# Optimization experiments

Hardware: AMD Instinct MI355X
Metric: run time of the kernel (lower is better)

Reference implementation:

```python
import jax, jax.numpy as jnp
import numpy as np

N = 8192      # num nodes
D = 128       # feature dim (input_dim)
E = 262144    # num edges (avg degree 32)
P = 4         # num perspectives (num_pers)
EPSILON = 0.3 # similarity threshold (args.epsilon)


def setup_inputs() -> dict:
    key = jax.random.key(0)
    k1, k2, k3, k4 = jax.random.split(key, 4)
    x = jax.random.normal(k1, (N, D), dtype=jnp.float32)
    ori_index = jax.random.randint(k2, (2, E), 0, N, dtype=jnp.int32)
    ori_weight = jax.random.uniform(k3, (E,), dtype=jnp.float32)
    w_pers = jax.random.normal(k4, (P, D), dtype=jnp.float32)  # weighted-cosine perspective weights
    return {"x": x, "ori_index": ori_index, "ori_weight": ori_weight, "w_pers": w_pers}


def reference(x, ori_index, ori_weight, w_pers):
    n = x.shape[0]
    # to_dense_adj: scatter edge weights into dense [N, N] adjacency (duplicate edges add)
    ori_g = jnp.zeros((n, n), dtype=x.dtype).at[ori_index[0], ori_index[1]].add(ori_weight)

    # GraphLearner (weighted multi-perspective cosine):
    # reweight features per perspective, L2-normalize, cosine sim, mean over perspectives
    xw = x[None, :, :] * w_pers[:, None, :]                              # [P, N, D]
    xn = xw / jnp.maximum(jnp.linalg.norm(xw, axis=-1, keepdims=True), 1e-12)
    sim = jnp.mean(jnp.einsum('pnd,pmd->pnm', xn, xn), axis=0)           # [N, N]
    # epsilon-thresholded learned graph
    sim_g = jnp.where(sim > EPSILON, sim, jnp.zeros_like(sim))

    # purified(sim, ori_g, epsilon): keep original edges where sim*ori_g > epsilon
    pur_g = jnp.where(sim * ori_g > EPSILON, ori_g, jnp.zeros_like(sim))
    new_g = pur_g + sim_g
    # dense_to_sparse has data-dependent output size; return the dense refined
    # adjacency (same information: edges = nonzero(new_g), weights = values).
    return new_g
```

## Files before the change

kernel.cpp:

```cpp
#include <hip/hip_runtime.h>
#include <hip/hip_bf16.h>
#include <stdint.h>

#define N_NODES 8192
#define DIM     128
#define KTOT    512
#define NEDGE   262144
#define EPS     0.3f
#define FIX_DELTA 0.008f
#define FIX_CAP (1u << 19)
#define XCAP    (1u << 18)
#define LCAP    512
#define HASH_BITS 19
#define HASH_SLOTS (1u << HASH_BITS)

typedef unsigned int u32;
typedef unsigned short u16;
typedef __attribute__((ext_vector_type(8))) short short8;
typedef __attribute__((ext_vector_type(4))) float float4v;

#define OFF_YF  0u
#define OFF_YB  16777216u
#define OFF_CTR 25165824u
#define OFF_HK  25166080u
#define OFF_HV  27263232u
#define OFF_FL  29360384u
#define OFF_UL  31457536u
#define OFF_XL  32506112u
#define MEMSET_OFF OFF_CTR
#define MEMSET_BYTES (OFF_FL - OFF_CTR)

__device__ __forceinline__ u16 f2bf(float f) {
    u32 b = __builtin_bit_cast(u32, f);
    b += 0x7fffu + ((b >> 16) & 1u);
    return (u16)(b >> 16);
}

__global__ void prep_y(const float* __restrict__ x, const float* __restrict__ wp,
                       float* __restrict__ yf, u16* __restrict__ yb) {
    int node = blockIdx.x * 4 + (threadIdx.x >> 6);
    int lane = threadIdx.x & 63;
    float x0 = x[node * DIM + lane];
    float x1 = x[node * DIM + lane + 64];
    for (int p = 0; p < 4; ++p) {
        float v0 = x0 * wp[p * DIM + lane];
        float v1 = x1 * wp[p * DIM + lane + 64];
        float ss = v0 * v0 + v1 * v1;
        #pragma unroll
        for (int o = 1; o < 64; o <<= 1) ss += __shfl_xor(ss, o, 64);
        float scale = 0.5f / fmaxf(sqrtf(ss), 1e-12f);
        float y0 = v0 * scale, y1 = v1 * scale;
        int base = node * KTOT + p * DIM;
        yf[base + lane] = y0;       yf[base + lane + 64] = y1;
        yb[base + lane] = f2bf(y0); yb[base + lane + 64] = f2bf(y1);
    }
}

__global__ void edge_insert(const int* __restrict__ idx, const float* __restrict__ w,
                            u32* __restrict__ hkey, float* __restrict__ hval,
                            u32* __restrict__ ucnt, u32* __restrict__ ulist) {
    int e = blockIdx.x * 256 + threadIdx.x;
    u32 cell = (u32)(idx[e] * N_NODES + idx[NEDGE + e]);
    float wv = w[e];
    u32 key = cell + 1u;
    u32 h = (cell * 2654435761u) >> (32 - HASH_BITS);
    while (true) {
        u32 old = atomicCAS(&hkey[h], 0u, key);
        if (old == 0u) { ulist[atomicAdd(ucnt, 1u)] = h; atomicAdd(&hval[h], wv); break; }
        if (old == key) { atomicAdd(&hval[h], wv); break; }
        h = (h + 1u) & (HASH_SLOTS - 1u);
    }
}

#define TM  128
#define BK  64
#define TLD 132

__global__ __launch_bounds__(512)
void gemm_sim(const u16* __restrict__ yb, float* __restrict__ out,
              u32* __restrict__ fcnt, u32* __restrict__ flst) {
    int bm = blockIdx.y, bn = blockIdx.x;
    if (bm > bn) return;
    __shared__ __align__(16) char smem[64 * TLD * 4];
    u16* As = (u16*)smem;
    u16* Bs = As + TM * BK;
    float* tbuf = (float*)smem;
    __shared__ u32 s_cnt, s_base;
    __shared__ u32 s_list[LCAP];
    int tid = threadIdx.x;
    int lane = tid & 63, wid = tid >> 6;
    int wm = wid >> 1, wn = wid & 1;
    if (tid == 0) s_cnt = 0;

    float4v acc[2][4] = {};
    const u16* arow = yb + (size_t)(bm * TM) * KTOT;
    const u16* brow = yb + (size_t)(bn * TM) * KTOT;

    for (int kt = 0; kt < KTOT / BK; ++kt) {
        __syncthreads();
        #pragma unroll
        for (int q = 0; q < 2; ++q) {
            int c = q * 512 + wid * 64 + lane;
            int row = c >> 3;
            int kg = (c & 7) ^ (row & 7);
            __builtin_amdgcn_global_load_lds(
                (const __attribute__((address_space(1))) void*)(const void*)(arow + (size_t)row * KTOT + kt * BK + kg * 8),
                (__attribute__((address_space(3))) void*)(void*)(As + (q * 512 + wid * 64) * 8),
                16, 0, 0);
            __builtin_amdgcn_global_load_lds(
                (const __attribute__((address_space(1))) void*)(const void*)(brow + (size_t)row * KTOT + kt * BK + kg * 8),
                (__attribute__((address_space(3))) void*)(void*)(Bs + (q * 512 + wid * 64) * 8),
                16, 0, 0);
        }
        __syncthreads();
        #pragma unroll
        for (int kk = 0; kk < 2; ++kk) {
            short8 af[2], bfr[4];
            int kg2 = kk * 4 + (lane >> 4);
            int mrow = wm * 32 + (lane & 15);
            int ncol = wn * 64 + (lane & 15);
            #pragma unroll
            for (int i = 0; i < 2; ++i) {
                int ra = mrow + i * 16;
                af[i] = *(const short8*)&As[ra * BK + ((kg2 ^ (ra & 7)) * 8)];
            }
            #pragma unroll
            for (int j = 0; j < 4; ++j) {
                int rb = ncol + j * 16;
                bfr[j] = *(const short8*)&Bs[rb * BK + ((kg2 ^ (rb & 7)) * 8)];
            }
            #pragma unroll
            for (int i = 0; i < 2; ++i)
                #pragma unroll
                for (int j = 0; j < 4; ++j)
                    acc[i][j] = __builtin_amdgcn_mfma_f32_16x16x32_bf16(
                        af[i], bfr[j], acc[i][j], 0, 0, 0);
        }
    }

    int quad = lane >> 4, lcol = lane & 15;
    #pragma unroll
    for (int i = 0; i < 2; ++i)
        #pragma unroll
        for (int j = 0; j < 4; ++j) {
            int gr0 = bm * TM + wm * 32 + i * 16 + quad * 4;
            int gc  = bn * TM + wn * 64 + j * 16 + lcol;
            #pragma unroll
            for (int r = 0; r < 4; ++r) {
                float s = acc[i][j][r];
                out[(size_t)(gr0 + r) * N_NODES + gc] = s > EPS ? s : 0.f;
                if (fabsf(s - EPS) < FIX_DELTA) {
                    u32 cell = (u32)((gr0 + r) * N_NODES + gc);
                    u32 li = atomicAdd(&s_cnt, 1u);
                    if (li < LCAP) s_list[li] = cell;
                    else { u32 g = atomicAdd(fcnt, 1u); if (g < FIX_CAP) flst[g] = cell; }
                }
            }
        }

    #pragma unroll
    for (int h = 0; h < 2; ++h) {
        __syncthreads();
        if (wn == h) {
            #pragma unroll
            for (int i = 0; i < 2; ++i) {
                int Lr = wm * 32 + i * 16 + quad * 4;
                #pragma unroll
                for (int j = 0; j < 4; ++j) {
                    int Lc = j * 16 + lcol;
                    *(float4v*)&tbuf[Lc * TLD + Lr] = acc[i][j];
                }
            }
        }
        __syncthreads();
        #pragma unroll
        for (int v = 0; v < 4; ++v) {
            int chunk = v * 512 + tid;
            int row = chunk >> 5, c4 = chunk & 31;
            float4v t = *(const float4v*)&tbuf[row * TLD + c4 * 4];
            float4v o;
            #pragma unroll
            for (int r = 0; r < 4; ++r) o[r] = t[r] > EPS ? t[r] : 0.f;
            *(float4v*)&out[(size_t)(bn * TM + h * 64 + row) * N_NODES + bm * TM + c4 * 4] = o;
        }
    }

    __syncthreads();
    u32 cnt = s_cnt < LCAP ? s_cnt : LCAP;
    if (tid == 0) s_base = atomicAdd(fcnt, cnt);
    __syncthreads();
    for (u32 t = tid; t < cnt; t += 512) {
        u32 g = s_base + t;
        if (g < FIX_CAP) flst[g] = s_list[t];
    }
}

__device__ __forceinline__ float dot_exact(const float* __restrict__ yf,
                                           u32 i, u32 j, int tl) {
    const float4v* ri = (const float4v*)(yf + (size_t)i * KTOT);
    const float4v* rj = (const float4v*)(yf + (size_t)j * KTOT);
    float4v p = {};
    #pragma unroll
    for (int q = 0; q < 8; ++q) p += ri[q * 16 + tl] * rj[q * 16 + tl];
    float s = p.x + p.y + p.z + p.w;
    #pragma unroll
    for (int o = 8; o >= 1; o >>= 1) s += __shfl_xor(s, o, 16);
    return s;
}

__global__ void fixup(const float* __restrict__ yf, const u32* __restrict__ fcnt,
                      const u32* __restrict__ flst, float* __restrict__ out) {
    u32 count = *fcnt; if (count > FIX_CAP) count = FIX_CAP;
    int team = (blockIdx.x * 256 + threadIdx.x) >> 4;
    int tl = threadIdx.x & 15;
    int nteams = gridDim.x * 16;
    for (u32 t = team; t < count; t += nteams) {
        u32 cell = flst[t];
        u32 i = cell >> 13, j = cell & 8191u;
        float s = dot_exact(yf, i, j, tl);
        if (tl == 0) {
            float v = s > EPS ? s : 0.f;
            out[(size_t)i * N_NODES + j] = v;
            out[(size_t)j * N_NODES + i] = v;
        }
    }
}

__global__ void edge_fast(const u32* __restrict__ hkey, const float* __restrict__ hval,
                          const u32* __restrict__ ucnt, const u32* __restrict__ ulist,
                          float* __restrict__ out,
                          u32* __restrict__ xcnt, u32* __restrict__ xlist) {
    u32 count = *ucnt;
    for (u32 t = blockIdx.x * 256 + threadIdx.x; t < count; t += gridDim.x * 256) {
        u32 h = ulist[t];
        u32 cell = hkey[h] - 1u;
        float a = hval[h];
        float sg = out[cell];
        bool hard = (a > 1.0f) ||
                    (sg > 0.f && fabsf(sg * a - EPS) < FIX_DELTA * a + 1e-6f) ||
                    (sg == 0.f && a > 0.97f);
        if (hard) {
            u32 g = atomicAdd(xcnt, 1u);
            if (g < XCAP) xlist[g] = h;
        } else if (sg > 0.f) {
            out[cell] = sg + ((sg * a > EPS) ? a : 0.f);
        }
    }
}

__global__ void edge_exact(const float* __restrict__ yf, const u32* __restrict__ hkey,
                           const float* __restrict__ hval, const u32* __restrict__ xcnt,
                           const u32* __restrict__ xlist, float* __restrict__ out) {
    u32 count = *xcnt; if (count > XCAP) count = XCAP;
    int team = (blockIdx.x * 256 + threadIdx.x) >> 4;
    int tl = threadIdx.x & 15;
    int nteams = gridDim.x * 16;
    for (u32 t = team; t < count; t += nteams) {
        u32 h = xlist[t];
        u32 cell = hkey[h] - 1u;
        float a = hval[h];
        u32 i = cell >> 13, j = cell & 8191u;
        float s = dot_exact(yf, i, j, tl);
        if (tl == 0) {
            float v = s > EPS ? s : 0.f;
            if (s * a > EPS) v += a;
            out[cell] = v;
        }
    }
}

extern "C" void kernel_launch(void* const* d_in, const int* in_sizes, int n_in,
                              void* d_out, int out_size, void* d_ws, size_t ws_size,
                              hipStream_t stream) {
    const float* x  = (const float*)d_in[0];
    const int*   oi = (const int*)d_in[1];
    const float* ow = (const float*)d_in[2];
    const float* wp = (const float*)d_in[3];
    float* out = (float*)d_out;
    char* ws = (char*)d_ws;
    float* yf = (float*)(ws + OFF_YF);
    u16*   yb = (u16*)(ws + OFF_YB);
    u32*   fc = (u32*)(ws + OFF_CTR);
    u32*   uc = (u32*)(ws + OFF_CTR + 4);
    u32*   xc = (u32*)(ws + OFF_CTR + 8);
    u32*   hk = (u32*)(ws + OFF_HK);
    float* hv = (float*)(ws + OFF_HV);
    u32*   fl = (u32*)(ws + OFF_FL);
    u32*   ul = (u32*)(ws + OFF_UL);
    u32*   xl = (u32*)(ws + OFF_XL);

    prep_y<<<N_NODES / 4, 256, 0, stream>>>(x, wp, yf, yb);
    hipMemsetAsync(ws + MEMSET_OFF, 0, MEMSET_BYTES, stream);
    edge_insert<<<NEDGE / 256, 256, 0, stream>>>(oi, ow, hk, hv, uc, ul);
    gemm_sim<<<dim3(N_NODES / TM, N_NODES / TM), 512, 0, stream>>>(yb, out, fc, fl);
    fixup<<<2048, 256, 0, stream>>>(yf, fc, fl, out);
    edge_fast<<<1024, 256, 0, stream>>>(hk, hv, uc, ul, out, xc, xl);
    edge_exact<<<256, 256, 0, stream>>>(yf, hk, hv, xc, xl, out);
}
```

Measured before the change: 488.7 us.

## Fuse memset into prep, merge fixup with edge pass, use nontemporal output stores

The workspace memset is folded into extra blocks of prep_y. The fixup and edge_fast kernels are merged into one launch with block-range dispatch, and the GEMM output stores become nontemporal. The fixup band is narrowed, and the edge pass gains an extra hard-case test for values near epsilon, because the two now run concurrently and edge_fast may read a cell before fixup rewrites it. This removes launch overhead and leaves more bandwidth for the dense output write, but the narrower band means fewer bf16 near-threshold cells are rechecked exactly.

After: 468.6 us, median of 2. -4.1%, faster.

```diff
diff --git a/kernel.cpp b/kernel.cpp
--- a/kernel.cpp
+++ b/kernel.cpp
@@ -7,7 +7,7 @@
 #define KTOT    512
 #define NEDGE   262144
 #define EPS     0.3f
-#define FIX_DELTA 0.008f
+#define FIX_DELTA 0.0043f
 #define FIX_CAP (1u << 19)
 #define XCAP    (1u << 18)
 #define LCAP    512
@@ -27,8 +27,7 @@
 #define OFF_FL  29360384u
 #define OFF_UL  31457536u
 #define OFF_XL  32506112u
-#define MEMSET_OFF OFF_CTR
-#define MEMSET_BYTES (OFF_FL - OFF_CTR)
+#define ZERO_VEC4 262160u
 
 __device__ __forceinline__ u16 f2bf(float f) {
     u32 b = __builtin_bit_cast(u32, f);
@@ -37,7 +36,14 @@
 }
 
 __global__ void prep_y(const float* __restrict__ x, const float* __restrict__ wp,
-                       float* __restrict__ yf, u16* __restrict__ yb) {
+                       float* __restrict__ yf, u16* __restrict__ yb,
+                       uint4* __restrict__ zbase) {
+    if (blockIdx.x >= 2048) {
+        for (u32 idx = (blockIdx.x - 2048) * 256 + threadIdx.x; idx < ZERO_VEC4;
+             idx += 512 * 256)
+            zbase[idx] = make_uint4(0, 0, 0, 0);
+        return;
+    }
     int node = blockIdx.x * 4 + (threadIdx.x >> 6);
     int lane = threadIdx.x & 63;
     float x0 = x[node * DIM + lane];
@@ -148,7 +154,8 @@
             #pragma unroll
             for (int r = 0; r < 4; ++r) {
                 float s = acc[i][j][r];
-                out[(size_t)(gr0 + r) * N_NODES + gc] = s > EPS ? s : 0.f;
+                __builtin_nontemporal_store(s > EPS ? s : 0.f,
+                                            &out[(size_t)(gr0 + r) * N_NODES + gc]);
                 if (fabsf(s - EPS) < FIX_DELTA) {
                     u32 cell = (u32)((gr0 + r) * N_NODES + gc);
                     u32 li = atomicAdd(&s_cnt, 1u);
@@ -181,7 +188,8 @@
             float4v o;
             #pragma unroll
             for (int r = 0; r < 4; ++r) o[r] = t[r] > EPS ? t[r] : 0.f;
-            *(float4v*)&out[(size_t)(bn * TM + h * 64 + row) * N_NODES + bm * TM + c4 * 4] = o;
+            __builtin_nontemporal_store(o,
+                (float4v*)&out[(size_t)(bn * TM + h * 64 + row) * N_NODES + bm * TM + c4 * 4]);
         }
     }
 
@@ -208,42 +216,44 @@
     return s;
 }
 
-__global__ void fixup(const float* __restrict__ yf, const u32* __restrict__ fcnt,
-                      const u32* __restrict__ flst, float* __restrict__ out) {
-    u32 count = *fcnt; if (count > FIX_CAP) count = FIX_CAP;
-    int team = (blockIdx.x * 256 + threadIdx.x) >> 4;
-    int tl = threadIdx.x & 15;
-    int nteams = gridDim.x * 16;
-    for (u32 t = team; t < count; t += nteams) {
-        u32 cell = flst[t];
-        u32 i = cell >> 13, j = cell & 8191u;
-        float s = dot_exact(yf, i, j, tl);
-        if (tl == 0) {
-            float v = s > EPS ? s : 0.f;
-            out[(size_t)i * N_NODES + j] = v;
-            out[(size_t)j * N_NODES + i] = v;
-        }
-    }
-}
-
-__global__ void edge_fast(const u32* __restrict__ hkey, const float* __restrict__ hval,
-                          const u32* __restrict__ ucnt, const u32* __restrict__ ulist,
-                          float* __restrict__ out,
-                          u32* __restrict__ xcnt, u32* __restrict__ xlist) {
-    u32 count = *ucnt;
-    for (u32 t = blockIdx.x * 256 + threadIdx.x; t < count; t += gridDim.x * 256) {
-        u32 h = ulist[t];
-        u32 cell = hkey[h] - 1u;
-        float a = hval[h];
-        float sg = out[cell];
-        bool hard = (a > 1.0f) ||
-                    (sg > 0.f && fabsf(sg * a - EPS) < FIX_DELTA * a + 1e-6f) ||
-                    (sg == 0.f && a > 0.97f);
-        if (hard) {
-            u32 g = atomicAdd(xcnt, 1u);
-            if (g < XCAP) xlist[g] = h;
-        } else if (sg > 0.f) {
-            out[cell] = sg + ((sg * a > EPS) ? a : 0.f);
+__global__ void fix_and_edges(const float* __restrict__ yf,
+                              const u32* __restrict__ fcnt, const u32* __restrict__ flst,
+                              const u32* __restrict__ hkey, const float* __restrict__ hval,
+                              const u32* __restrict__ ucnt, const u32* __restrict__ ulist,
+                              float* __restrict__ out,
+                              u32* __restrict__ xcnt, u32* __restrict__ xlist) {
+    if (blockIdx.x < 1024) {
+        u32 count = *fcnt; if (count > FIX_CAP) count = FIX_CAP;
+        int team = (blockIdx.x * 256 + threadIdx.x) >> 4;
+        int tl = threadIdx.x & 15;
+        int nteams = 1024 * 16;
+        for (u32 t = team; t < count; t += nteams) {
+            u32 cell = flst[t];
+            u32 i = cell >> 13, j = cell & 8191u;
+            float s = dot_exact(yf, i, j, tl);
+            if (tl == 0) {
+                float v = s > EPS ? s : 0.f;
+                out[(size_t)i * N_NODES + j] = v;
+                out[(size_t)j * N_NODES + i] = v;
+            }
+        }
+    } else {
+        u32 count = *ucnt;
+        for (u32 t = (blockIdx.x - 1024) * 256 + threadIdx.x; t < count; t += 512 * 256) {
+            u32 h = ulist[t];
+            u32 cell = hkey[h] - 1u;
+            float a = hval[h];
+            float sg = out[cell];
+            bool hard = (a > 1.0f) ||
+                        (fabsf(sg - EPS) < FIX_DELTA + 1e-6f) ||
+                        (sg > 0.f && fabsf(sg * a - EPS) < FIX_DELTA * a + 1e-6f) ||
+                        (sg == 0.f && a > 0.97f);
+            if (hard) {
+                u32 g = atomicAdd(xcnt, 1u);
+                if (g < XCAP) xlist[g] = h;
+            } else if (sg > 0.f) {
+                out[cell] = sg + ((sg * a > EPS) ? a : 0.f);
+            }
         }
     }
 }
@@ -289,11 +299,9 @@
     u32*   ul = (u32*)(ws + OFF_UL);
     u32*   xl = (u32*)(ws + OFF_XL);
 
-    prep_y<<<N_NODES / 4, 256, 0, stream>>>(x, wp, yf, yb);
-    hipMemsetAsync(ws + MEMSET_OFF, 0, MEMSET_BYTES, stream);
+    prep_y<<<2560, 256, 0, stream>>>(x, wp, yf, yb, (uint4*)(ws + OFF_CTR));
     edge_insert<<<NEDGE / 256, 256, 0, stream>>>(oi, ow, hk, hv, uc, ul);
     gemm_sim<<<dim3(N_NODES / TM, N_NODES / TM), 512, 0, stream>>>(yb, out, fc, fl);
-    fixup<<<2048, 256, 0, stream>>>(yf, fc, fl, out);
-    edge_fast<<<1024, 256, 0, stream>>>(hk, hv, uc, ul, out, xc, xl);
+    fix_and_edges<<<1536, 256, 0, stream>>>(yf, fc, fl, hk, hv, uc, ul, out, xc, xl);
     edge_exact<<<256, 256, 0, stream>>>(yf, hk, hv, xc, xl, out);
 }
```
